# Kernel optimization log

Measured on AMD Instinct MI355X. Metric: run time of the kernel, lower is better.

## Reference

```python
import jax, jax.numpy as jnp
import numpy as np

N, K, R = 32768, 4096, 256

def setup_inputs() -> dict:
    key = jax.random.key(0)
    k1, k2, k3 = jax.random.split(key, 3)
    H = jax.random.normal(k1, (N, R), dtype=jnp.float32)
    L = jax.random.normal(k2, (K, R), dtype=jnp.float32)
    W_I = jax.random.normal(k3, (R, R), dtype=jnp.float32)
    return {"H": H, "L": L, "W_I": W_I}

def reference(H, L, W_I):
    # Q = W_I @ L^T : (r, k)
    Q = jnp.einsum('rs,ks->rk', W_I, L)
    # M_I = H @ Q : (n, k)
    M_I = jnp.einsum('nr,rk->nk', H, Q)
    A_I = jax.nn.softmax(M_I, axis=1)
    # C_I = A_I @ L : (n, r)
    C_I = jnp.einsum('nk,kr->nr', A_I, L)
    return (C_I, A_I)
```

## Files before the change

kernel.cpp:

```cpp
#include <hip/hip_runtime.h>
#include <hip/hip_bf16.h>
#include <math.h>
#include <stdint.h>

constexpr int N_ROWS = 32768;
constexpr int K_DIM  = 4096;
constexpr int R_DIM  = 256;
constexpr int KP     = 3 * R_DIM;
constexpr int KB     = K_DIM / 128;

typedef __bf16 bf16x8 __attribute__((ext_vector_type(8)));
typedef float  f32x4  __attribute__((ext_vector_type(4)));
typedef unsigned short u16x8 __attribute__((ext_vector_type(8)));
typedef unsigned short u16x4 __attribute__((ext_vector_type(4)));

__device__ __forceinline__ unsigned short f2bf(float x) {
    unsigned u = __float_as_uint(x);
    u += 0x7fffu + ((u >> 16) & 1u);
    return (unsigned short)(u >> 16);
}
__device__ __forceinline__ float bf2f(unsigned short h) {
    return __uint_as_float((unsigned)h << 16);
}

__device__ __forceinline__ void gl2lds16(const void* gptr, void* lptr) {
    __builtin_amdgcn_global_load_lds(
        (const __attribute__((address_space(1))) unsigned int*)gptr,
        (__attribute__((address_space(3))) unsigned int*)lptr,
        16, 0, 0);
}

__global__ __launch_bounds__(256)
void gemm_mfma_nt(const unsigned short* __restrict__ A,
                  const unsigned short* __restrict__ B,
                  float* __restrict__ C,
                  float* __restrict__ Pm, float* __restrict__ Ps,
                  int M, int N, int Kc)
{
    __shared__ __align__(16) unsigned short As[128 * 32];
    __shared__ __align__(16) unsigned short Bs[128 * 32];
    __shared__ float pm_s[128][2], ps_s[128][2];

    const int tid  = threadIdx.x;
    const int wave = tid >> 6, lane = tid & 63;
    const int wm = wave >> 1, wn = wave & 1;

    const int bid = blockIdx.x;
    const int xg = bid >> 10;
    const int yb = (bid >> 5) & 31;
    const int xi = bid & 31;
    const long m0 = (long)(xg * 32 + xi) * 128;
    const long n0 = (long)yb * 128;

    f32x4 acc[4][4] = {};

    const int srow  = lane >> 2;
    const int skoff = (lane & 3) * 8;
    const int c0 = wave, c1 = wave + 4;
    const int kq = (lane >> 4) * 8;
    const int mr = lane & 15;

    for (int k0 = 0; k0 < Kc; k0 += 32) {
        gl2lds16(A + (m0 + c0 * 16 + srow) * (long)Kc + k0 + skoff, &As[c0 * 512]);
        gl2lds16(A + (m0 + c1 * 16 + srow) * (long)Kc + k0 + skoff, &As[c1 * 512]);
        gl2lds16(B + (n0 + c0 * 16 + srow) * (long)Kc + k0 + skoff, &Bs[c0 * 512]);
        gl2lds16(B + (n0 + c1 * 16 + srow) * (long)Kc + k0 + skoff, &Bs[c1 * 512]);
        __syncthreads();

        bf16x8 af[4], bfr[4];
#pragma unroll
        for (int t = 0; t < 4; ++t) {
            af[t]  = *(const bf16x8*)&As[(wm * 64 + t * 16 + mr) * 32 + kq];
            bfr[t] = *(const bf16x8*)&Bs[(wn * 64 + t * 16 + mr) * 32 + kq];
        }
#pragma unroll
        for (int i = 0; i < 4; ++i)
#pragma unroll
            for (int j = 0; j < 4; ++j)
                acc[i][j] = __builtin_amdgcn_mfma_f32_16x16x32_bf16(
                    af[i], bfr[j], acc[i][j], 0, 0, 0);
        __syncthreads();
    }

    const int col = lane & 15, rquad = (lane >> 4) * 4;
#pragma unroll
    for (int i = 0; i < 4; ++i) {
        const long mrow = m0 + wm * 64 + i * 16 + rquad;
#pragma unroll
        for (int j = 0; j < 4; ++j) {
            float* p = C + mrow * (long)N + n0 + wn * 64 + j * 16 + col;
#pragma unroll
            for (int r = 0; r < 4; ++r) p[(long)r * N] = acc[i][j][r];
        }
    }

#pragma unroll
    for (int i = 0; i < 4; ++i) {
#pragma unroll
        for (int r = 0; r < 4; ++r) {
            float mx = fmaxf(fmaxf(acc[i][0][r], acc[i][1][r]),
                             fmaxf(acc[i][2][r], acc[i][3][r]));
#pragma unroll
            for (int off = 1; off < 16; off <<= 1)
                mx = fmaxf(mx, __shfl_xor(mx, off));
            float sm = 0.f;
#pragma unroll
            for (int j = 0; j < 4; ++j) sm += __expf(acc[i][j][r] - mx);
#pragma unroll
            for (int off = 1; off < 16; off <<= 1)
                sm += __shfl_xor(sm, off);
            if (mr == 0) {
                const int rw = wm * 64 + i * 16 + rquad + r;
                pm_s[rw][wn] = mx;
                ps_s[rw][wn] = sm;
            }
        }
    }
    __syncthreads();
    if (tid < 128) {
        const float ma = pm_s[tid][0], mb = pm_s[tid][1];
        const float mx = fmaxf(ma, mb);
        const float s  = ps_s[tid][0] * __expf(ma - mx) +
                         ps_s[tid][1] * __expf(mb - mx);
        Pm[(m0 + tid) * KB + yb] = mx;
        Ps[(m0 + tid) * KB + yb] = s;
    }
}

__global__ __launch_bounds__(256)
void finalize_ms(const float* __restrict__ Pm, const float* __restrict__ Ps,
                 float* __restrict__ SMm, float* __restrict__ SMi)
{
    const long row = (long)blockIdx.x * 256 + threadIdx.x;
    const float4* pm = (const float4*)(Pm + row * KB);
    const float4* ps = (const float4*)(Ps + row * KB);
    float4 v[8];
    float mx = -3.4e38f;
#pragma unroll
    for (int q = 0; q < 8; ++q) {
        v[q] = pm[q];
        mx = fmaxf(mx, fmaxf(fmaxf(v[q].x, v[q].y), fmaxf(v[q].z, v[q].w)));
    }
    float s = 0.f;
#pragma unroll
    for (int q = 0; q < 8; ++q) {
        float4 w = ps[q];
        s += w.x * __expf(v[q].x - mx) + w.y * __expf(v[q].y - mx) +
             w.z * __expf(v[q].z - mx) + w.w * __expf(v[q].w - mx);
    }
    SMm[row] = mx;
    SMi[row] = 1.f / s;
}

__global__ __launch_bounds__(512)
void softmax_av_pv(float* __restrict__ Mio,
                   const unsigned short* __restrict__ LT,
                   const float* __restrict__ SMm, const float* __restrict__ SMi,
                   float* __restrict__ C)
{
    __shared__ __align__(16) unsigned short Bs[R_DIM * 64];
    __shared__ __align__(16) unsigned short As[64 * 64];
    __shared__ float sm_m[64], sm_inv[64];

    const int tid  = threadIdx.x;
    const int wave = tid >> 6, lane = tid & 63;
    const long m0 = (long)blockIdx.x * 64;

    if (tid < 64) { sm_m[tid] = SMm[m0 + tid]; sm_inv[tid] = SMi[m0 + tid]; }
    __syncthreads();

    f32x4 acc[2][4] = {};
    const int wm = wave >> 2, wn = wave & 3;
    const int mr = lane & 15;
    const int kq16 = (lane >> 4) * 16;

    const int arow0 = wave * 4 + (lane >> 4);
    const int arow1 = 32 + arow0;
    const int acolE = (lane & 15) * 4;
    float* const gp0 = Mio + (m0 + arow0) * (long)K_DIM + acolE;
    float* const gp1 = Mio + (m0 + arow1) * (long)K_DIM + acolE;
    const int ab0 = (arow0 * 128 + acolE * 2) ^ ((arow0 & 7) << 4);
    const int ab1 = (arow1 * 128 + acolE * 2) ^ ((arow1 & 7) << 4);
    const float mm0 = sm_m[arow0], ii0 = sm_inv[arow0];
    const float mm1 = sm_m[arow1], ii1 = sm_inv[arow1];

    float4 va0 = *(const float4*)gp0;
    float4 va1 = *(const float4*)gp1;

    for (int t = 0; t < K_DIM / 64; ++t) {
        const int k0 = t * 64;
#pragma unroll
        for (int q = 0; q < 4; ++q) {
            const int rbase = q * 64 + wave * 8;
            const int rloc  = rbase + (lane >> 3);
            const int phys  = (lane & 7) * 16;
            const int kbyte = phys ^ ((rloc & 7) << 4);
            gl2lds16((const char*)LT + (long)rloc * (K_DIM * 2) + (long)k0 * 2 + kbyte,
                     &Bs[rbase * 64]);
        }
        {
            float e0 = __expf(va0.x - mm0), e1 = __expf(va0.y - mm0);
            float e2 = __expf(va0.z - mm0), e3 = __expf(va0.w - mm0);
            *(float4*)(gp0 + k0) = make_float4(e0 * ii0, e1 * ii0, e2 * ii0, e3 * ii0);
            u16x4 u0; u0[0] = f2bf(e0); u0[1] = f2bf(e1); u0[2] = f2bf(e2); u0[3] = f2bf(e3);
            *(u16x4*)((char*)As + ab0) = u0;

            float f0 = __expf(va1.x - mm1), f1 = __expf(va1.y - mm1);
            float f2 = __expf(va1.z - mm1), f3 = __expf(va1.w - mm1);
            *(float4*)(gp1 + k0) = make_float4(f0 * ii1, f1 * ii1, f2 * ii1, f3 * ii1);
            u16x4 u1; u1[0] = f2bf(f0); u1[1] = f2bf(f1); u1[2] = f2bf(f2); u1[3] = f2bf(f3);
            *(u16x4*)((char*)As + ab1) = u1;
        }
        __syncthreads();

        if (t + 1 < K_DIM / 64) {
            va0 = *(const float4*)(gp0 + k0 + 64);
            va1 = *(const float4*)(gp1 + k0 + 64);
        }

#pragma unroll
        for (int ks = 0; ks < 2; ++ks) {
            bf16x8 af[2], bfr[4];
#pragma unroll
            for (int tt = 0; tt < 2; ++tt) {
                const int arow = wm * 32 + tt * 16 + mr;
                const int ab = (arow * 128 + ks * 64 + kq16) ^ ((arow & 7) << 4);
                af[tt] = *(const bf16x8*)((const char*)As + ab);
            }
#pragma unroll
            for (int tt = 0; tt < 4; ++tt) {
                const int brow = wn * 64 + tt * 16 + mr;
                const int bb = (brow * 128 + ks * 64 + kq16) ^ ((brow & 7) << 4);
                bfr[tt] = *(const bf16x8*)((const char*)Bs + bb);
            }
#pragma unroll
            for (int i = 0; i < 2; ++i)
#pragma unroll
                for (int j = 0; j < 4; ++j)
                    acc[i][j] = __builtin_amdgcn_mfma_f32_16x16x32_bf16(
                        af[i], bfr[j], acc[i][j], 0, 0, 0);
        }
        __syncthreads();
    }

    const int col = lane & 15, rquad = (lane >> 4) * 4;
#pragma unroll
    for (int i = 0; i < 2; ++i) {
        const int lrow0 = wm * 32 + i * 16 + rquad;
#pragma unroll
        for (int j = 0; j < 4; ++j) {
            float* p = C + (m0 + lrow0) * (long)R_DIM + wn * 64 + j * 16 + col;
#pragma unroll
            for (int r = 0; r < 4; ++r)
                p[(long)r * R_DIM] = acc[i][j][r] * sm_inv[lrow0 + r];
        }
    }
}

__global__ __launch_bounds__(256)
void prep_B(const float* __restrict__ L, unsigned short* __restrict__ Bp)
{
    const long i = (long)blockIdx.x * 256 + threadIdx.x;
    const long k = i >> 8; const int r = (int)(i & 255);
    const float x = L[i];
    const unsigned short hi = f2bf(x);
    const unsigned short lo = f2bf(x - bf2f(hi));
    unsigned short* row = Bp + k * KP;
    row[r] = hi; row[R_DIM + r] = lo; row[2 * R_DIM + r] = hi;
}

__global__ __launch_bounds__(256)
void prep_LT(const float* __restrict__ L, unsigned short* __restrict__ LT)
{
    const long i = (long)blockIdx.x * 256 + threadIdx.x;
    const long r = i >> 12; const long k = i & 4095;
    LT[r * K_DIM + k] = f2bf(L[k * R_DIM + r]);
}

template<bool BT>
__global__ __launch_bounds__(256)
void gemm128(const float* __restrict__ A, const float* __restrict__ B,
             float* __restrict__ C, int M, int N, int Kc)
{
    __shared__ __align__(16) float Asl[16][132];
    __shared__ __align__(16) float Bsl[16][132];

    const int tid = threadIdx.x;
    const int tx = tid & 15, ty = tid >> 4;
    const long m0 = (long)blockIdx.x * 128;
    const long n0 = (long)blockIdx.y * 128;

    float acc[8][8];
#pragma unroll
    for (int i = 0; i < 8; ++i)
#pragma unroll
        for (int j = 0; j < 8; ++j) acc[i][j] = 0.f;

    for (int k0 = 0; k0 < Kc; k0 += 16) {
#pragma unroll
        for (int q = 0; q < 2; ++q) {
            int fi = tid + 256 * q, row = fi >> 2, col = (fi & 3) * 4;
            float4 v = *(const float4*)(A + (m0 + row) * (long)Kc + k0 + col);
            Asl[col + 0][row] = v.x; Asl[col + 1][row] = v.y;
            Asl[col + 2][row] = v.z; Asl[col + 3][row] = v.w;
        }
        if (BT) {
#pragma unroll
            for (int q = 0; q < 2; ++q) {
                int fi = tid + 256 * q, row = fi >> 2, col = (fi & 3) * 4;
                float4 v = *(const float4*)(B + (n0 + row) * (long)Kc + k0 + col);
                Bsl[col + 0][row] = v.x; Bsl[col + 1][row] = v.y;
                Bsl[col + 2][row] = v.z; Bsl[col + 3][row] = v.w;
            }
        } else {
#pragma unroll
            for (int q = 0; q < 2; ++q) {
                int fi = tid + 256 * q, row = fi >> 5, col = (fi & 31) * 4;
                float4 v = *(const float4*)(B + (k0 + row) * (long)N + n0 + col);
                *(float4*)&Bsl[row][col] = v;
            }
        }
        __syncthreads();
#pragma unroll
        for (int kk = 0; kk < 16; ++kk) {
            float a[8], b[8];
            *(float4*)&a[0] = *(const float4*)&Asl[kk][ty * 8];
            *(float4*)&a[4] = *(const float4*)&Asl[kk][ty * 8 + 4];
            *(float4*)&b[0] = *(const float4*)&Bsl[kk][tx * 8];
            *(float4*)&b[4] = *(const float4*)&Bsl[kk][tx * 8 + 4];
#pragma unroll
            for (int i = 0; i < 8; ++i)
#pragma unroll
                for (int j = 0; j < 8; ++j)
                    acc[i][j] = fmaf(a[i], b[j], acc[i][j]);
        }
        __syncthreads();
    }
#pragma unroll
    for (int i = 0; i < 8; ++i) {
        float* p = C + (m0 + ty * 8 + i) * (long)N + n0 + tx * 8;
        *(float4*)p       = make_float4(acc[i][0], acc[i][1], acc[i][2], acc[i][3]);
        *(float4*)(p + 4) = make_float4(acc[i][4], acc[i][5], acc[i][6], acc[i][7]);
    }
}

__global__ __launch_bounds__(256)
void gemm128_hl(const float* __restrict__ A, const float* __restrict__ B,
                unsigned short* __restrict__ Ap, int M, int N, int Kc)
{
    __shared__ __align__(16) float Asl[16][132];
    __shared__ __align__(16) float Bsl[16][132];

    const int tid = threadIdx.x;
    const int tx = tid & 15, ty = tid >> 4;
    const long m0 = (long)blockIdx.x * 128;
    const long n0 = (long)blockIdx.y * 128;

    float acc[8][8];
#pragma unroll
    for (int i = 0; i < 8; ++i)
#pragma unroll
        for (int j = 0; j < 8; ++j) acc[i][j] = 0.f;

    for (int k0 = 0; k0 < Kc; k0 += 16) {
#pragma unroll
        for (int q = 0; q < 2; ++q) {
            int fi = tid + 256 * q, row = fi >> 2, col = (fi & 3) * 4;
            float4 v = *(const float4*)(A + (m0 + row) * (long)Kc + k0 + col);
            Asl[col + 0][row] = v.x; Asl[col + 1][row] = v.y;
            Asl[col + 2][row] = v.z; Asl[col + 3][row] = v.w;
        }
#pragma unroll
        for (int q = 0; q < 2; ++q) {
            int fi = tid + 256 * q, row = fi >> 5, col = (fi & 31) * 4;
            float4 v = *(const float4*)(B + (k0 + row) * (long)N + n0 + col);
            *(float4*)&Bsl[row][col] = v;
        }
        __syncthreads();
#pragma unroll
        for (int kk = 0; kk < 16; ++kk) {
            float a[8], b[8];
            *(float4*)&a[0] = *(const float4*)&Asl[kk][ty * 8];
            *(float4*)&a[4] = *(const float4*)&Asl[kk][ty * 8 + 4];
            *(float4*)&b[0] = *(const float4*)&Bsl[kk][tx * 8];
            *(float4*)&b[4] = *(const float4*)&Bsl[kk][tx * 8 + 4];
#pragma unroll
            for (int i = 0; i < 8; ++i)
#pragma unroll
                for (int j = 0; j < 8; ++j)
                    acc[i][j] = fmaf(a[i], b[j], acc[i][j]);
        }
        __syncthreads();
    }
#pragma unroll
    for (int i = 0; i < 8; ++i) {
        const long row = m0 + ty * 8 + i;
        const int  cb  = (int)n0 + tx * 8;
        u16x8 vh, vl;
#pragma unroll
        for (int j = 0; j < 8; ++j) {
            const float x = acc[i][j];
            const unsigned short hi = f2bf(x);
            vh[j] = hi;
            vl[j] = f2bf(x - bf2f(hi));
        }
        unsigned short* rp = Ap + row * KP;
        *(u16x8*)(rp + cb)             = vh;
        *(u16x8*)(rp + R_DIM + cb)     = vh;
        *(u16x8*)(rp + 2 * R_DIM + cb) = vl;
    }
}

__global__ __launch_bounds__(256)
void softmax_rows(float* __restrict__ Mio)
{
    const long n  = blockIdx.x;
    float* row    = Mio + n * (long)K_DIM;
    const int tid = threadIdx.x;

    float4 v[4];
    float lmax = -3.4e38f;
#pragma unroll
    for (int q = 0; q < 4; ++q) {
        v[q] = ((const float4*)row)[tid + 256 * q];
        lmax = fmaxf(lmax, fmaxf(fmaxf(v[q].x, v[q].y), fmaxf(v[q].z, v[q].w)));
    }
    __shared__ float redmax[4], redsum[4];
#pragma unroll
    for (int off = 32; off > 0; off >>= 1)
        lmax = fmaxf(lmax, __shfl_xor(lmax, off));
    if ((tid & 63) == 0) redmax[tid >> 6] = lmax;
    __syncthreads();
    const float gmax = fmaxf(fmaxf(redmax[0], redmax[1]), fmaxf(redmax[2], redmax[3]));

    float lsum = 0.f;
#pragma unroll
    for (int q = 0; q < 4; ++q) {
        v[q].x = __expf(v[q].x - gmax); v[q].y = __expf(v[q].y - gmax);
        v[q].z = __expf(v[q].z - gmax); v[q].w = __expf(v[q].w - gmax);
        lsum += v[q].x + v[q].y + v[q].z + v[q].w;
    }
#pragma unroll
    for (int off = 32; off > 0; off >>= 1)
        lsum += __shfl_xor(lsum, off);
    if ((tid & 63) == 0) redsum[tid >> 6] = lsum;
    __syncthreads();
    const float inv = 1.f / (redsum[0] + redsum[1] + redsum[2] + redsum[3]);
#pragma unroll
    for (int q = 0; q < 4; ++q) {
        v[q].x *= inv; v[q].y *= inv; v[q].z *= inv; v[q].w *= inv;
        ((float4*)row)[tid + 256 * q] = v[q];
    }
}

extern "C" void kernel_launch(void* const* d_in, const int* in_sizes, int n_in,
                              void* d_out, int out_size, void* d_ws, size_t ws_size,
                              hipStream_t stream)
{
    const float* H  = (const float*)d_in[0];
    const float* L  = (const float*)d_in[1];
    const float* Wi = (const float*)d_in[2];

    float* Cout = (float*)d_out;
    float* Aout = (float*)d_out + (size_t)N_ROWS * R_DIM;

    const size_t szAp = (size_t)N_ROWS * KP * 2;
    const size_t szBp = (size_t)K_DIM * KP * 2;
    const size_t szLT = (size_t)R_DIM * K_DIM * 2;
    const size_t szPm = (size_t)N_ROWS * KB * 4;
    const size_t szPs = (size_t)N_ROWS * KB * 4;
    const size_t szSM = (size_t)N_ROWS * 4;

    if (ws_size >= szAp + szBp + szLT + szPm + szPs + 2 * szSM) {
        char* w = (char*)d_ws;
        unsigned short* Ap = (unsigned short*)w;                 w += szAp;
        unsigned short* Bp = (unsigned short*)w;                 w += szBp;
        unsigned short* LT = (unsigned short*)w;                 w += szLT;
        float* Pm  = (float*)w;                                  w += szPm;
        float* Ps  = (float*)w;                                  w += szPs;
        float* SMm = (float*)w;                                  w += szSM;
        float* SMi = (float*)w;

        gemm128_hl<<<dim3(N_ROWS / 128, R_DIM / 128), 256, 0, stream>>>(
            H, Wi, Ap, N_ROWS, R_DIM, R_DIM);
        prep_B<<<dim3((K_DIM * R_DIM) / 256), 256, 0, stream>>>(L, Bp);
        prep_LT<<<dim3((R_DIM * K_DIM) / 256), 256, 0, stream>>>(L, LT);
        gemm_mfma_nt<<<dim3((N_ROWS / 128) * (K_DIM / 128)), 256, 0, stream>>>(
            Ap, Bp, Aout, Pm, Ps, N_ROWS, K_DIM, KP);
        finalize_ms<<<dim3(N_ROWS / 256), 256, 0, stream>>>(Pm, Ps, SMm, SMi);
        softmax_av_pv<<<dim3(N_ROWS / 64), 512, 0, stream>>>(
            Aout, LT, SMm, SMi, Cout);
    } else {
        gemm128<false><<<dim3(N_ROWS / 128, R_DIM / 128), 256, 0, stream>>>(
            H, Wi, Cout, N_ROWS, R_DIM, R_DIM);
        gemm128<true><<<dim3(N_ROWS / 128, K_DIM / 128), 256, 0, stream>>>(
            Cout, L, Aout, N_ROWS, K_DIM, R_DIM);
        softmax_rows<<<dim3(N_ROWS), 256, 0, stream>>>(Aout);
        gemm128<false><<<dim3(N_ROWS / 128, R_DIM / 128), 256, 0, stream>>>(
            Aout, L, Cout, N_ROWS, R_DIM, K_DIM);
    }
}
```

Before: 1.205 ms.

## Store block-local exp logits as bf16 in upper half of output buffer

The logits GEMM now writes exp(logit - block max) as bf16 into the second half of each output row instead of writing fp32 logits. The softmax/PV kernel reads these bf16 values and rescales them with a per-128-column correction factor built from Pm, SMm and SMi. This halves the intermediate write and read traffic and moves the exp work out of the second kernel. The cost is bf16 rounding of the probabilities, and a carefully placed barrier before the last tile so the in-place fp32 writes do not overwrite bf16 data that has not been read yet.

```diff
diff --git a/kernel.cpp b/kernel.cpp
--- a/kernel.cpp
+++ b/kernel.cpp
@@ -33,13 +33,14 @@
 __global__ __launch_bounds__(256)
 void gemm_mfma_nt(const unsigned short* __restrict__ A,
                   const unsigned short* __restrict__ B,
-                  float* __restrict__ C,
+                  float* __restrict__ Mout,
                   float* __restrict__ Pm, float* __restrict__ Ps,
                   int M, int N, int Kc)
 {
     __shared__ __align__(16) unsigned short As[128 * 32];
     __shared__ __align__(16) unsigned short Bs[128 * 32];
     __shared__ float pm_s[128][2], ps_s[128][2];
+    __shared__ float pmc[128];
 
     const int tid  = threadIdx.x;
     const int wave = tid >> 6, lane = tid & 63;
@@ -83,16 +84,6 @@
     }
 
     const int col = lane & 15, rquad = (lane >> 4) * 4;
-#pragma unroll
-    for (int i = 0; i < 4; ++i) {
-        const long mrow = m0 + wm * 64 + i * 16 + rquad;
-#pragma unroll
-        for (int j = 0; j < 4; ++j) {
-            float* p = C + mrow * (long)N + n0 + wn * 64 + j * 16 + col;
-#pragma unroll
-            for (int r = 0; r < 4; ++r) p[(long)r * N] = acc[i][j][r];
-        }
-    }
 
 #pragma unroll
     for (int i = 0; i < 4; ++i) {
@@ -122,8 +113,25 @@
         const float mx = fmaxf(ma, mb);
         const float s  = ps_s[tid][0] * __expf(ma - mx) +
                          ps_s[tid][1] * __expf(mb - mx);
+        pmc[tid] = mx;
         Pm[(m0 + tid) * KB + yb] = mx;
         Ps[(m0 + tid) * KB + yb] = s;
+    }
+    __syncthreads();
+
+    unsigned short* E = (unsigned short*)Mout;
+#pragma unroll
+    for (int i = 0; i < 4; ++i) {
+#pragma unroll
+        for (int r = 0; r < 4; ++r) {
+            const int rw = wm * 64 + i * 16 + rquad + r;
+            const float mx = pmc[rw];
+            unsigned short* ep =
+                E + (m0 + rw) * 8192L + 4096 + n0 + wn * 64 + col;
+#pragma unroll
+            for (int j = 0; j < 4; ++j)
+                ep[j * 16] = f2bf(__expf(acc[i][j][r] - mx));
+        }
     }
 }
 
@@ -153,20 +161,32 @@
 }
 
 __global__ __launch_bounds__(512)
-void softmax_av_pv(float* __restrict__ Mio,
+void softmax_av_pv(float* Aout,
                    const unsigned short* __restrict__ LT,
-                   const float* __restrict__ SMm, const float* __restrict__ SMi,
+                   const float* __restrict__ Pm,
+                   const float* __restrict__ SMm,
+                   const float* __restrict__ SMi,
                    float* __restrict__ C)
 {
     __shared__ __align__(16) unsigned short Bs[R_DIM * 64];
     __shared__ __align__(16) unsigned short As[64 * 64];
-    __shared__ float sm_m[64], sm_inv[64];
+    __shared__ float cs[64][32];
 
     const int tid  = threadIdx.x;
     const int wave = tid >> 6, lane = tid & 63;
     const long m0 = (long)blockIdx.x * 64;
 
-    if (tid < 64) { sm_m[tid] = SMm[m0 + tid]; sm_inv[tid] = SMi[m0 + tid]; }
+    {
+        const int i0 = tid * 4;
+        const int r  = i0 >> 5;
+        const int b  = i0 & 31;
+        const float m = SMm[m0 + r], inv = SMi[m0 + r];
+        const float4 pv = *(const float4*)(Pm + (m0 + r) * KB + b);
+        cs[r][b + 0] = __expf(pv.x - m) * inv;
+        cs[r][b + 1] = __expf(pv.y - m) * inv;
+        cs[r][b + 2] = __expf(pv.z - m) * inv;
+        cs[r][b + 3] = __expf(pv.w - m) * inv;
+    }
     __syncthreads();
 
     f32x4 acc[2][4] = {};
@@ -177,18 +197,23 @@
     const int arow0 = wave * 4 + (lane >> 4);
     const int arow1 = 32 + arow0;
     const int acolE = (lane & 15) * 4;
-    float* const gp0 = Mio + (m0 + arow0) * (long)K_DIM + acolE;
-    float* const gp1 = Mio + (m0 + arow1) * (long)K_DIM + acolE;
+    const unsigned short* const ep0 =
+        (const unsigned short*)Aout + (m0 + arow0) * 8192L + 4096 + acolE;
+    const unsigned short* const ep1 =
+        (const unsigned short*)Aout + (m0 + arow1) * 8192L + 4096 + acolE;
+    float* const gp0 = Aout + (m0 + arow0) * (long)K_DIM + acolE;
+    float* const gp1 = Aout + (m0 + arow1) * (long)K_DIM + acolE;
     const int ab0 = (arow0 * 128 + acolE * 2) ^ ((arow0 & 7) << 4);
     const int ab1 = (arow1 * 128 + acolE * 2) ^ ((arow1 & 7) << 4);
-    const float mm0 = sm_m[arow0], ii0 = sm_inv[arow0];
-    const float mm1 = sm_m[arow1], ii1 = sm_inv[arow1];
-
-    float4 va0 = *(const float4*)gp0;
-    float4 va1 = *(const float4*)gp1;
-
-    for (int t = 0; t < K_DIM / 64; ++t) {
+
+    u16x4 va0 = *(const u16x4*)ep0;
+    u16x4 va1 = *(const u16x4*)ep1;
+
+    constexpr int NT = K_DIM / 64;
+    for (int t = 0; t < NT; ++t) {
         const int k0 = t * 64;
+        if (t == NT - 1) __syncthreads();
+
 #pragma unroll
         for (int q = 0; q < 4; ++q) {
             const int rbase = q * 64 + wave * 8;
@@ -199,23 +224,26 @@
                      &Bs[rbase * 64]);
         }
         {
-            float e0 = __expf(va0.x - mm0), e1 = __expf(va0.y - mm0);
-            float e2 = __expf(va0.z - mm0), e3 = __expf(va0.w - mm0);
-            *(float4*)(gp0 + k0) = make_float4(e0 * ii0, e1 * ii0, e2 * ii0, e3 * ii0);
-            u16x4 u0; u0[0] = f2bf(e0); u0[1] = f2bf(e1); u0[2] = f2bf(e2); u0[3] = f2bf(e3);
+            const float c0 = cs[arow0][t >> 1], c1 = cs[arow1][t >> 1];
+            float a0 = bf2f(va0[0]) * c0, a1 = bf2f(va0[1]) * c0;
+            float a2 = bf2f(va0[2]) * c0, a3 = bf2f(va0[3]) * c0;
+            *(float4*)(gp0 + k0) = make_float4(a0, a1, a2, a3);
+            u16x4 u0;
+            u0[0] = f2bf(a0); u0[1] = f2bf(a1); u0[2] = f2bf(a2); u0[3] = f2bf(a3);
             *(u16x4*)((char*)As + ab0) = u0;
 
-            float f0 = __expf(va1.x - mm1), f1 = __expf(va1.y - mm1);
-            float f2 = __expf(va1.z - mm1), f3 = __expf(va1.w - mm1);
-            *(float4*)(gp1 + k0) = make_float4(f0 * ii1, f1 * ii1, f2 * ii1, f3 * ii1);
-            u16x4 u1; u1[0] = f2bf(f0); u1[1] = f2bf(f1); u1[2] = f2bf(f2); u1[3] = f2bf(f3);
+            float b0 = bf2f(va1[0]) * c1, b1 = bf2f(va1[1]) * c1;
+            float b2 = bf2f(va1[2]) * c1, b3 = bf2f(va1[3]) * c1;
+            *(float4*)(gp1 + k0) = make_float4(b0, b1, b2, b3);
+            u16x4 u1;
+            u1[0] = f2bf(b0); u1[1] = f2bf(b1); u1[2] = f2bf(b2); u1[3] = f2bf(b3);
             *(u16x4*)((char*)As + ab1) = u1;
         }
         __syncthreads();
 
-        if (t + 1 < K_DIM / 64) {
-            va0 = *(const float4*)(gp0 + k0 + 64);
-            va1 = *(const float4*)(gp1 + k0 + 64);
+        if (t + 1 < NT) {
+            va0 = *(const u16x4*)(ep0 + (t + 1) * 64);
+            va1 = *(const u16x4*)(ep1 + (t + 1) * 64);
         }
 
 #pragma unroll
@@ -252,7 +280,7 @@
             float* p = C + (m0 + lrow0) * (long)R_DIM + wn * 64 + j * 16 + col;
 #pragma unroll
             for (int r = 0; r < 4; ++r)
-                p[(long)r * R_DIM] = acc[i][j][r] * sm_inv[lrow0 + r];
+                p[(long)r * R_DIM] = acc[i][j][r];
         }
     }
 }
@@ -489,7 +517,7 @@
             Ap, Bp, Aout, Pm, Ps, N_ROWS, K_DIM, KP);
         finalize_ms<<<dim3(N_ROWS / 256), 256, 0, stream>>>(Pm, Ps, SMm, SMi);
         softmax_av_pv<<<dim3(N_ROWS / 64), 512, 0, stream>>>(
-            Aout, LT, SMm, SMi, Cout);
+            Aout, LT, Pm, SMm, SMi, Cout);
     } else {
         gemm128<false><<<dim3(N_ROWS / 128, R_DIM / 128), 256, 0, stream>>>(
             H, Wi, Cout, N_ROWS, R_DIM, R_DIM);
```

Result: faster. 1.150 ms (-4.6%).
